# Performance work log

Measured on AMD Instinct MI355X. Metric: run time of the kernel, lower is better.

## Reference

```python
import jax, jax.numpy as jnp
import numpy as np

VDIM, HDIM, B = 128, 512, 512
EPS = 1e-5  # torch LayerNorm default


def _ln(x, g, b):
    m = x.mean(-1, keepdims=True)
    v = ((x - m) ** 2).mean(-1, keepdims=True)
    return (x - m) * jax.lax.rsqrt(v + EPS) * g + b


def setup_inputs() -> dict:
    key = jax.random.key(0)
    ks = jax.random.split(key, 16)
    s = 0.05  # small init so sigmoids/logs stay numerically tame
    d = {}
    d["u"] = jax.random.uniform(ks[0], (VDIM, B), jnp.float32)
    d["q_w1"] = s * jax.random.normal(ks[1], (VDIM, HDIM), jnp.float32)
    d["q_b1"] = jnp.zeros((HDIM,), jnp.float32)
    d["q_g1"] = jnp.ones((HDIM,), jnp.float32)
    d["q_be1"] = jnp.zeros((HDIM,), jnp.float32)
    d["q_w2"] = s * jax.random.normal(ks[2], (HDIM, HDIM), jnp.float32)
    d["q_b2"] = jnp.zeros((HDIM,), jnp.float32)
    d["q_g2"] = jnp.ones((HDIM,), jnp.float32)
    d["q_be2"] = jnp.zeros((HDIM,), jnp.float32)
    d["q_w3"] = s * jax.random.normal(ks[3], (HDIM, HDIM), jnp.float32)
    d["q_b3"] = jnp.zeros((HDIM,), jnp.float32)
    d["q_g3"] = jnp.ones((HDIM,), jnp.float32)
    d["q_be3"] = jnp.zeros((HDIM,), jnp.float32)
    d["q_W"] = 0.01 * jax.random.normal(ks[4], (VDIM, HDIM), jnp.float32)  # per-node output heads
    d["q_bias"] = jnp.zeros((VDIM,), jnp.float32)
    d["q_marg"] = jnp.zeros((VDIM,), jnp.float32)
    d["f_w1"] = s * jax.random.normal(ks[5], (VDIM, HDIM), jnp.float32)
    d["f_b1"] = jnp.zeros((HDIM,), jnp.float32)
    d["f_g1"] = jnp.ones((HDIM,), jnp.float32)
    d["f_be1"] = jnp.zeros((HDIM,), jnp.float32)
    d["f_w2"] = s * jax.random.normal(ks[6], (HDIM, HDIM), jnp.float32)
    d["f_b2"] = jnp.zeros((HDIM,), jnp.float32)
    d["f_g2"] = jnp.ones((HDIM,), jnp.float32)
    d["f_be2"] = jnp.zeros((HDIM,), jnp.float32)
    d["f_w3"] = s * jax.random.normal(ks[7], (HDIM, HDIM), jnp.float32)
    d["f_b3"] = jnp.zeros((HDIM,), jnp.float32)
    d["f_g3"] = jnp.ones((HDIM,), jnp.float32)
    d["f_be3"] = jnp.zeros((HDIM,), jnp.float32)
    d["f_w4"] = s * jax.random.normal(ks[8], (HDIM,), jnp.float32)
    d["f_b4"] = jnp.zeros((1,), jnp.float32)
    d["J"] = 0.1 * jax.random.normal(ks[9], (VDIM, VDIM), jnp.float32)  # Ising couplings for scorer
    d["top_order"] = jnp.arange(VDIM, dtype=jnp.int32)
    d["pa_mask"] = jax.random.randint(ks[10], (VDIM, VDIM), 0, 2, jnp.int32)
    return d


def reference(u, q_w1, q_b1, q_g1, q_be1, q_w2, q_b2, q_g2, q_be2,
              q_w3, q_b3, q_g3, q_be3, q_W, q_bias, q_marg,
              f_w1, f_b1, f_g1, f_be1, f_w2, f_b2, f_g2, f_be2,
              f_w3, f_b3, f_g3, f_be3, f_w4, f_b4, J,
              top_order, pa_mask):
    def qtrunk(V):
        h = jax.nn.relu(_ln(V @ q_w1 + q_b1, q_g1, q_be1))
        h = jax.nn.relu(_ln(h @ q_w2 + q_b2, q_g2, q_be2))
        h = jax.nn.relu(_ln(h @ q_w3 + q_b3, q_g3, q_be3))
        return h  # [B, H]

    def fnet(V):
        h = jax.nn.relu(_ln(V @ f_w1 + f_b1, f_g1, f_be1))
        h = jax.nn.relu(_ln(h @ f_w2 + f_b2, f_g2, f_be2))
        h = jax.nn.relu(_ln(h @ f_w3 + f_b3, f_g3, f_be3))
        return h @ f_w4 + f_b4[0]  # [B]

    # gather per-node quantities in topological order once, outside the scan
    masks = pa_mask[top_order].astype(u.dtype)          # [V, V] parent masks
    Wq = q_W[top_order]                                  # [V, H]
    bq = q_bias[top_order]                               # [V]
    mg = q_marg[top_order]                               # [V]
    oh = jax.nn.one_hot(top_order, VDIM, dtype=u.dtype)  # [V, V]

    def step(V, xs):
        mask_i, Wq_i, bq_i, mg_i, oh_i, u_i = xs
        V_pa = V * mask_i                                # [B, V] parents only
        x = qtrunk(V_pa) @ Wq_i + bq_i                   # [B]
        empty = jnp.abs(V_pa).sum(1) == 0
        p_on = jnp.where(empty, jax.nn.sigmoid(mg_i), jax.nn.sigmoid(x))
        samp = u_i < p_on                                # bernoulli(p_on)
        v_samp = 2.0 * samp.astype(u.dtype) - 1.0
        V_new = V * (1.0 - oh_i) + v_samp[:, None] * oh_i  # scatter into column
        lp = jnp.where(samp, jnp.log(p_on), jnp.log1p(-p_on))
        logF = fnet(jax.lax.stop_gradient(V_new))        # V.clone().detach()
        return V_new, (lp, logF)

    V0 = jnp.zeros((B, VDIM), u.dtype)
    V, (lps, logFs) = jax.lax.scan(step, V0, (masks, Wq, bq, mg, oh, u))
    log_pf = lps.T                                       # [B, V]
    F0 = fnet(V0)                                        # log_flow[:, 0] (alg='db')
    score = jax.lax.stop_gradient(jnp.einsum('bi,ij,bj->b', V, J, V))  # -energy, detached
    # last logF is overwritten by the terminal score, as in the original
    log_flow = jnp.concatenate([F0[:, None], logFs[:-1].T, score[:, None]], axis=1)  # [B, V+1]
    loss = ((log_flow[:, :-1] + log_pf - log_flow[:, 1:]) ** 2).mean(1).mean()
    return V, loss
```

## Files before the change

kernel.cpp:

```cpp
#include <hip/hip_runtime.h>
#include <hip/hip_bf16.h>
#include <math.h>

#define VDIM 128
#define HDIM 512
#define BATCH 512
#define RPB 4
#define NBLK (BATCH / RPB)
#define NWORK 128
#define NT 512
#define NWAVE 8
#define LN_EPS 1e-5f
#define FROWS 32
#define NGRP (BATCH / FROWS)
#define SBPG (FROWS / RPB)

__device__ __forceinline__ float4 f4zero() { return make_float4(0.f, 0.f, 0.f, 0.f); }
__device__ __forceinline__ float4 f4add(float4 a, float4 b) {
    return make_float4(a.x + b.x, a.y + b.y, a.z + b.z, a.w + b.w);
}
__device__ __forceinline__ float4 f4fma(float4 a, float s, float4 c) {
    return make_float4(fmaf(a.x, s, c.x), fmaf(a.y, s, c.y),
                       fmaf(a.z, s, c.z), fmaf(a.w, s, c.w));
}
__device__ __forceinline__ float4 f4scale(float4 a, float s) {
    return make_float4(a.x * s, a.y * s, a.z * s, a.w * s);
}
__device__ __forceinline__ float4 f4sub(float4 a, float4 b) {
    return make_float4(a.x - b.x, a.y - b.y, a.z - b.z, a.w - b.w);
}
__device__ __forceinline__ float f4get(float4 v, int r) {
    return r == 0 ? v.x : r == 1 ? v.y : r == 2 ? v.z : v.w;
}

struct Params {
    const float *u;
    const float *q_w1, *q_b1, *q_g1, *q_be1;
    const float *q_w2, *q_b2, *q_g2, *q_be2;
    const float *q_w3, *q_b3, *q_g3, *q_be3;
    const float *q_W, *q_bias, *q_marg;
    const float *f_w1, *f_b1, *f_g1, *f_be1;
    const float *f_w2, *f_b2, *f_g2, *f_be2;
    const float *f_w3, *f_b3, *f_g3, *f_be3;
    const float *f_w4, *f_b4, *J;
    const int *top_order, *pa_mask;
    int *flag;
    float *V_out, *lp, *lf, *score, *vs, *loss;
};

struct ScanS {
    float4 VT[VDIM];
    float4 VPT[VDIM];
    float4 ATa[HDIM];
    float4 ATb[HDIM];
    float4 part[4][4][128];
    float4 redA[NWAVE], redB[NWAVE];
};
struct WorkS {
    float Vt[VDIM * FROWS];
    float A[HDIM * FROWS];
    int ord[VDIM], invp[VDIM];
    float4 redA[NWAVE], redB[NWAVE];
};
union SMem { ScanS s; WorkS w; };

__device__ __forceinline__ float4 allreduce4_1s(float4 v, float4 *red, int tid) {
#pragma unroll
    for (int off = 1; off < 64; off <<= 1) {
        v.x += __shfl_xor(v.x, off, 64);
        v.y += __shfl_xor(v.y, off, 64);
        v.z += __shfl_xor(v.z, off, 64);
        v.w += __shfl_xor(v.w, off, 64);
    }
    if ((tid & 63) == 0) red[tid >> 6] = v;
    __syncthreads();
    float4 s = red[0];
#pragma unroll
    for (int w = 1; w < NWAVE; ++w) s = f4add(s, red[w]);
    return s;
}

__device__ __forceinline__ float block_reduce1(float v, float *red, int tid) {
#pragma unroll
    for (int off = 1; off < 64; off <<= 1) v += __shfl_xor(v, off, 64);
    if ((tid & 63) == 0) red[tid >> 6] = v;
    __syncthreads();
    float s = 0.f;
#pragma unroll
    for (int w = 0; w < NWAVE; ++w) s += red[w];
    __syncthreads();
    return s;
}

__device__ __forceinline__ void redpair(float4 &a, float4 &b,
                                        float4 *redA, float4 *redB, int tid) {
#pragma unroll
    for (int off = 1; off < 64; off <<= 1) {
        a.x += __shfl_xor(a.x, off, 64); a.y += __shfl_xor(a.y, off, 64);
        a.z += __shfl_xor(a.z, off, 64); a.w += __shfl_xor(a.w, off, 64);
        b.x += __shfl_xor(b.x, off, 64); b.y += __shfl_xor(b.y, off, 64);
        b.z += __shfl_xor(b.z, off, 64); b.w += __shfl_xor(b.w, off, 64);
    }
    int w = tid >> 6;
    if ((tid & 63) == 0) { redA[w] = a; redB[w] = b; }
    __syncthreads();
    int p = w ^ 1;
    a = f4add(redA[w], redA[p]);
    b = f4add(redB[w], redB[p]);
    __syncthreads();
}

template <int K>
__device__ __forceinline__ void gemv_ln_scan(const float4 *__restrict__ inA,
                                             const float *__restrict__ W,
                                             const float *__restrict__ bias,
                                             const float *__restrict__ gam,
                                             const float *__restrict__ bet,
                                             float4 *__restrict__ outA,
                                             ScanS &S, int tid, int ks, int cq,
                                             int myc) {
    constexpr int kc = K / 4;
    constexpr int q4 = kc / 4;
    constexpr int seg = K / 4;
    const float4 *Wp = (const float4 *)W + (size_t)(ks * kc) * (HDIM / 4) + cq;
    const float4 *ap = inA + ks * q4;
    float4 acc0 = f4zero(), acc1 = f4zero(), acc2 = f4zero(), acc3 = f4zero();
#pragma unroll 4
    for (int q = 0; q < q4; ++q) {
        float4 a0 = ap[q];
        float4 a1 = ap[q + seg];
        float4 a2 = ap[q + 2 * seg];
        float4 a3 = ap[q + 3 * seg];
        float4 w0 = Wp[(size_t)(4 * q + 0) * (HDIM / 4)];
        float4 w1 = Wp[(size_t)(4 * q + 1) * (HDIM / 4)];
        float4 w2 = Wp[(size_t)(4 * q + 2) * (HDIM / 4)];
        float4 w3 = Wp[(size_t)(4 * q + 3) * (HDIM / 4)];
        acc0 = f4fma(a0, w0.x, acc0); acc1 = f4fma(a0, w0.y, acc1);
        acc2 = f4fma(a0, w0.z, acc2); acc3 = f4fma(a0, w0.w, acc3);
        acc0 = f4fma(a1, w1.x, acc0); acc1 = f4fma(a1, w1.y, acc1);
        acc2 = f4fma(a1, w1.z, acc2); acc3 = f4fma(a1, w1.w, acc3);
        acc0 = f4fma(a2, w2.x, acc0); acc1 = f4fma(a2, w2.y, acc1);
        acc2 = f4fma(a2, w2.z, acc2); acc3 = f4fma(a2, w2.w, acc3);
        acc0 = f4fma(a3, w3.x, acc0); acc1 = f4fma(a3, w3.y, acc1);
        acc2 = f4fma(a3, w3.z, acc2); acc3 = f4fma(a3, w3.w, acc3);
    }
    S.part[0][ks][cq] = acc0;
    S.part[1][ks][cq] = acc1;
    S.part[2][ks][cq] = acc2;
    S.part[3][ks][cq] = acc3;
    __syncthreads();
    const int j = ks, cb = cq;
    float4 acc = f4add(f4add(S.part[j][0][cb], S.part[j][1][cb]),
                       f4add(S.part[j][2][cb], S.part[j][3][cb]));
    float bc = bias[myc];
    acc.x += bc; acc.y += bc; acc.z += bc; acc.w += bc;
    const float inv = 1.f / (float)HDIM;
    float4 m4 = f4scale(allreduce4_1s(acc, S.redA, tid), inv);
    float4 d = f4sub(acc, m4);
    float4 sq = make_float4(d.x * d.x, d.y * d.y, d.z * d.z, d.w * d.w);
    float4 var = f4scale(allreduce4_1s(sq, S.redB, tid), inv);
    float4 rs;
    rs.x = 1.f / sqrtf(var.x + LN_EPS);
    rs.y = 1.f / sqrtf(var.y + LN_EPS);
    rs.z = 1.f / sqrtf(var.z + LN_EPS);
    rs.w = 1.f / sqrtf(var.w + LN_EPS);
    float gc = gam[myc], ec = bet[myc];
    float4 h;
    h.x = fmaxf(fmaf(d.x * rs.x, gc, ec), 0.f);
    h.y = fmaxf(fmaf(d.y * rs.y, gc, ec), 0.f);
    h.z = fmaxf(fmaf(d.z * rs.z, gc, ec), 0.f);
    h.w = fmaxf(fmaf(d.w * rs.w, gc, ec), 0.f);
    outA[tid] = h;
    __syncthreads();
}

__device__ void scan_role(const Params &P, int bid, ScanS &S) {
    const int tid = threadIdx.x;
    const int ks = tid >> 7;
    const int cq = tid & 127;
    const int myc = 4 * cq + ks;
    const int row0 = bid * RPB;

    if (tid < VDIM) S.VT[tid] = f4zero();
    __syncthreads();

    for (int i = 0; i < VDIM; ++i) {
        const int node = P.top_order[i];

        float4 apv = f4zero();
        if (tid < VDIM) {
            float mk = (float)P.pa_mask[node * VDIM + tid];
            float4 vp = f4scale(S.VT[tid], mk);
            S.VPT[(tid & 3) * 32 + (tid >> 2)] = vp;
            apv = make_float4(fabsf(vp.x), fabsf(vp.y), fabsf(vp.z), fabsf(vp.w));
        }
        float4 asum = allreduce4_1s(apv, S.redB, tid);

        gemv_ln_scan<VDIM>(S.VPT, P.q_w1, P.q_b1, P.q_g1, P.q_be1, S.ATa, S, tid, ks, cq, myc);
        gemv_ln_scan<HDIM>(S.ATa, P.q_w2, P.q_b2, P.q_g2, P.q_be2, S.ATb, S, tid, ks, cq, myc);
        gemv_ln_scan<HDIM>(S.ATb, P.q_w3, P.q_b3, P.q_g3, P.q_be3, S.ATa, S, tid, ks, cq, myc);

        float wq = P.q_W[(size_t)node * HDIM + myc];
        float4 x4 = allreduce4_1s(f4scale(S.ATa[tid], wq), S.redA, tid);

        if (tid < RPB) {
            const int r = tid;
            float asr = f4get(asum, r);
            float xr = f4get(x4, r) + P.q_bias[node];
            float arg = (asr == 0.f) ? P.q_marg[node] : xr;
            float p = 1.f / (1.f + expf(-arg));
            float uv = P.u[i * BATCH + row0 + r];
            bool samp = uv < p;
            float v = samp ? 1.f : -1.f;
            ((float *)&S.VT[node])[r] = v;
            __hip_atomic_store(&P.vs[(size_t)i * BATCH + row0 + r], v,
                               __ATOMIC_RELAXED, __HIP_MEMORY_SCOPE_AGENT);
            P.lp[(size_t)i * BATCH + row0 + r] = samp ? logf(p) : log1pf(-p);
        }
        __syncthreads();
        if (tid == 0) {
            __hip_atomic_store(P.flag + bid, i + 1,
                               __ATOMIC_RELEASE, __HIP_MEMORY_SCOPE_AGENT);
        }
    }

    float4 inner = f4zero();
    if (tid < VDIM) {
#pragma unroll 4
        for (int ii = 0; ii < VDIM; ++ii)
            inner = f4fma(S.VT[ii], P.J[(size_t)ii * VDIM + tid], inner);
        float4 vc = S.VT[tid];
        inner = make_float4(inner.x * vc.x, inner.y * vc.y, inner.z * vc.z, inner.w * vc.w);
    }
    float4 sc4 = allreduce4_1s(inner, S.redA, tid);
    if (tid < RPB) P.score[row0 + tid] = f4get(sc4, tid);
    if (tid < VDIM) {
        float4 v = S.VT[tid];
        P.V_out[(size_t)(row0 + 0) * VDIM + tid] = v.x;
        P.V_out[(size_t)(row0 + 1) * VDIM + tid] = v.y;
        P.V_out[(size_t)(row0 + 2) * VDIM + tid] = v.z;
        P.V_out[(size_t)(row0 + 3) * VDIM + tid] = v.w;
    }
}

template <int K>
__device__ __forceinline__ void flayer512(const float *__restrict__ in,
                                          const float *__restrict__ W,
                                          const float *__restrict__ bias,
                                          const float *__restrict__ gam,
                                          const float *__restrict__ bet,
                                          float *__restrict__ out,
                                          float4 *redA, float4 *redB, int tid) {
    const int rh = tid >> 7;
    const int cq = tid & 127;
    const float4 *Wv = (const float4 *)W + cq;
    float4 accA[4], accB[4];
#pragma unroll
    for (int j = 0; j < 4; ++j) { accA[j] = f4zero(); accB[j] = f4zero(); }
#pragma unroll 4
    for (int k = 0; k < K; ++k) {
        float4 w = Wv[(size_t)k * (HDIM / 4)];
        const float *ip = in + k * FROWS + 8 * rh;
        float4 vA = *(const float4 *)ip;
        float4 vB = *(const float4 *)(ip + 4);
        accA[0] = f4fma(vA, w.x, accA[0]); accB[0] = f4fma(vB, w.x, accB[0]);
        accA[1] = f4fma(vA, w.y, accA[1]); accB[1] = f4fma(vB, w.y, accB[1]);
        accA[2] = f4fma(vA, w.z, accA[2]); accB[2] = f4fma(vB, w.z, accB[2]);
        accA[3] = f4fma(vA, w.w, accA[3]); accB[3] = f4fma(vB, w.w, accB[3]);
    }
    float4 b4 = ((const float4 *)bias)[cq];
    float bb[4] = {b4.x, b4.y, b4.z, b4.w};
#pragma unroll
    for (int j = 0; j < 4; ++j) {
        accA[j].x += bb[j]; accA[j].y += bb[j]; accA[j].z += bb[j]; accA[j].w += bb[j];
        accB[j].x += bb[j]; accB[j].y += bb[j]; accB[j].z += bb[j]; accB[j].w += bb[j];
    }
    const float inv = 1.f / (float)HDIM;
    float4 sA = f4add(f4add(accA[0], accA[1]), f4add(accA[2], accA[3]));
    float4 sB = f4add(f4add(accB[0], accB[1]), f4add(accB[2], accB[3]));
    redpair(sA, sB, redA, redB, tid);
    float4 mA = f4scale(sA, inv), mB = f4scale(sB, inv);
    float4 dA[4], dB[4];
    float4 qA = f4zero(), qB = f4zero();
#pragma unroll
    for (int j = 0; j < 4; ++j) {
        dA[j] = f4sub(accA[j], mA);
        dB[j] = f4sub(accB[j], mB);
        qA.x += dA[j].x * dA[j].x; qA.y += dA[j].y * dA[j].y;
        qA.z += dA[j].z * dA[j].z; qA.w += dA[j].w * dA[j].w;
        qB.x += dB[j].x * dB[j].x; qB.y += dB[j].y * dB[j].y;
        qB.z += dB[j].z * dB[j].z; qB.w += dB[j].w * dB[j].w;
    }
    redpair(qA, qB, redA, redB, tid);
    float4 rsA, rsB;
    rsA.x = 1.f / sqrtf(qA.x * inv + LN_EPS); rsA.y = 1.f / sqrtf(qA.y * inv + LN_EPS);
    rsA.z = 1.f / sqrtf(qA.z * inv + LN_EPS); rsA.w = 1.f / sqrtf(qA.w * inv + LN_EPS);
    rsB.x = 1.f / sqrtf(qB.x * inv + LN_EPS); rsB.y = 1.f / sqrtf(qB.y * inv + LN_EPS);
    rsB.z = 1.f / sqrtf(qB.z * inv + LN_EPS); rsB.w = 1.f / sqrtf(qB.w * inv + LN_EPS);
    float4 g4 = ((const float4 *)gam)[cq];
    float4 e4 = ((const float4 *)bet)[cq];
    float gg[4] = {g4.x, g4.y, g4.z, g4.w};
    float ee[4] = {e4.x, e4.y, e4.z, e4.w};
#pragma unroll
    for (int j = 0; j < 4; ++j) {
        float4 hA, hB;
        hA.x = fmaxf(fmaf(dA[j].x * rsA.x, gg[j], ee[j]), 0.f);
        hA.y = fmaxf(fmaf(dA[j].y * rsA.y, gg[j], ee[j]), 0.f);
        hA.z = fmaxf(fmaf(dA[j].z * rsA.z, gg[j], ee[j]), 0.f);
        hA.w = fmaxf(fmaf(dA[j].w * rsA.w, gg[j], ee[j]), 0.f);
        hB.x = fmaxf(fmaf(dB[j].x * rsB.x, gg[j], ee[j]), 0.f);
        hB.y = fmaxf(fmaf(dB[j].y * rsB.y, gg[j], ee[j]), 0.f);
        hB.z = fmaxf(fmaf(dB[j].z * rsB.z, gg[j], ee[j]), 0.f);
        hB.w = fmaxf(fmaf(dB[j].w * rsB.w, gg[j], ee[j]), 0.f);
        float *op = out + (4 * cq + j) * FROWS + 8 * rh;
        *(float4 *)op = hA;
        *(float4 *)(op + 4) = hB;
    }
    __syncthreads();
}

__device__ void worker_role(const Params &P, int wid, WorkS &S) {
    const int tid = threadIdx.x;
    if (tid < VDIM) S.ord[tid] = P.top_order[tid];
    __syncthreads();
    if (tid < VDIM) S.invp[S.ord[tid]] = tid;
    __syncthreads();
    const int g = wid & (NGRP - 1);
    const int r0 = g * FROWS;

    for (int tile = wid; tile < VDIM * NGRP; tile += NWORK) {
        const int t = tile >> 4;
        if (t == VDIM - 1) continue;
        if (tid < SBPG) {
            const int need = t + 1;
            while (__hip_atomic_load(P.flag + (SBPG * g + tid),
                                     __ATOMIC_RELAXED,
                                     __HIP_MEMORY_SCOPE_AGENT) < need)
                __builtin_amdgcn_s_sleep(4);
        }
        __syncthreads();
        for (int idx = tid; idx < VDIM * FROWS; idx += NT) {
            int k = idx >> 5, rr = idx & (FROWS - 1);
            int s = S.invp[k];
            S.Vt[idx] = (s <= t)
                ? __hip_atomic_load(&P.vs[(size_t)s * BATCH + r0 + rr],
                                    __ATOMIC_RELAXED, __HIP_MEMORY_SCOPE_AGENT)
                : 0.f;
        }
        __syncthreads();

        flayer512<VDIM>(S.Vt, P.f_w1, P.f_b1, P.f_g1, P.f_be1, S.A, S.redA, S.redB, tid);
        flayer512<HDIM>(S.A, P.f_w2, P.f_b2, P.f_g2, P.f_be2, S.A, S.redA, S.redB, tid);
        flayer512<HDIM>(S.A, P.f_w3, P.f_b3, P.f_g3, P.f_be3, S.A, S.redA, S.redB, tid);

        const int rh = tid >> 7, cq = tid & 127;
        float4 w4 = ((const float4 *)P.f_w4)[cq];
        float ww[4] = {w4.x, w4.y, w4.z, w4.w};
        float4 sA = f4zero(), sB = f4zero();
#pragma unroll
        for (int j = 0; j < 4; ++j) {
            const float *ap2 = S.A + (4 * cq + j) * FROWS + 8 * rh;
            float4 vA = *(const float4 *)ap2;
            float4 vB = *(const float4 *)(ap2 + 4);
            sA = f4fma(vA, ww[j], sA);
            sB = f4fma(vB, ww[j], sB);
        }
        redpair(sA, sB, S.redA, S.redB, tid);
        if (cq == 0) {
            float b4v = P.f_b4[0];
            float *dst = P.lf + (size_t)t * BATCH + r0 + 8 * rh;
            dst[0] = sA.x + b4v; dst[1] = sA.y + b4v;
            dst[2] = sA.z + b4v; dst[3] = sA.w + b4v;
            dst[4] = sB.x + b4v; dst[5] = sB.y + b4v;
            dst[6] = sB.z + b4v; dst[7] = sB.w + b4v;
        }
        __syncthreads();
    }
}

__global__ __launch_bounds__(NT) void gfn_main(Params P) {
    __shared__ SMem sm;
    const int xcd = blockIdx.x & 7;
    const int grp = blockIdx.x >> 3;
    if (xcd < 4) scan_role(P, grp * 4 + xcd, sm.s);
    else         worker_role(P, grp * 4 + (xcd - 4), sm.w);
}

__global__ __launch_bounds__(NT) void gfn_loss(Params P) {
    __shared__ float H1[HDIM], H2[HDIM];
    __shared__ float red1[NWAVE];
    const int tid = threadIdx.x;
    const float inv = 1.f / (float)HDIM;

    float z = P.f_b1[tid];
    float m = block_reduce1(z, red1, tid) * inv;
    float d = z - m;
    float var = block_reduce1(d * d, red1, tid) * inv;
    float h = fmaxf(fmaf(d * (1.f / sqrtf(var + LN_EPS)), P.f_g1[tid], P.f_be1[tid]), 0.f);
    H1[tid] = h;
    __syncthreads();

    float acc = 0.f;
    for (int k = 0; k < HDIM; ++k) acc = fmaf(H1[k], P.f_w2[(size_t)k * HDIM + tid], acc);
    z = acc + P.f_b2[tid];
    m = block_reduce1(z, red1, tid) * inv;
    d = z - m;
    var = block_reduce1(d * d, red1, tid) * inv;
    h = fmaxf(fmaf(d * (1.f / sqrtf(var + LN_EPS)), P.f_g2[tid], P.f_be2[tid]), 0.f);
    H2[tid] = h;
    __syncthreads();

    acc = 0.f;
    for (int k = 0; k < HDIM; ++k) acc = fmaf(H2[k], P.f_w3[(size_t)k * HDIM + tid], acc);
    z = acc + P.f_b3[tid];
    m = block_reduce1(z, red1, tid) * inv;
    d = z - m;
    var = block_reduce1(d * d, red1, tid) * inv;
    h = fmaxf(fmaf(d * (1.f / sqrtf(var + LN_EPS)), P.f_g3[tid], P.f_be3[tid]), 0.f);
    float F0 = block_reduce1(h * P.f_w4[tid], red1, tid) + P.f_b4[0];

    const int b = tid;
    float lfp = F0;
    float s = 0.f;
    for (int t = 0; t < VDIM; ++t) {
        float lp = P.lp[(size_t)t * BATCH + b];
        float lfn = (t == VDIM - 1) ? P.score[b] : P.lf[(size_t)t * BATCH + b];
        float dd = lfp + lp - lfn;
        s = fmaf(dd, dd, s);
        lfp = lfn;
    }
    s *= (1.f / (float)VDIM);
    float total = block_reduce1(s, red1, tid) * (1.f / (float)BATCH);
    if (tid == 0) P.loss[0] = total;
}

extern "C" void kernel_launch(void *const *d_in, const int *in_sizes, int n_in,
                              void *d_out, int out_size, void *d_ws, size_t ws_size,
                              hipStream_t stream) {
    Params P;
    P.u     = (const float *)d_in[0];
    P.q_w1  = (const float *)d_in[1];
    P.q_b1  = (const float *)d_in[2];
    P.q_g1  = (const float *)d_in[3];
    P.q_be1 = (const float *)d_in[4];
    P.q_w2  = (const float *)d_in[5];
    P.q_b2  = (const float *)d_in[6];
    P.q_g2  = (const float *)d_in[7];
    P.q_be2 = (const float *)d_in[8];
    P.q_w3  = (const float *)d_in[9];
    P.q_b3  = (const float *)d_in[10];
    P.q_g3  = (const float *)d_in[11];
    P.q_be3 = (const float *)d_in[12];
    P.q_W   = (const float *)d_in[13];
    P.q_bias= (const float *)d_in[14];
    P.q_marg= (const float *)d_in[15];
    P.f_w1  = (const float *)d_in[16];
    P.f_b1  = (const float *)d_in[17];
    P.f_g1  = (const float *)d_in[18];
    P.f_be1 = (const float *)d_in[19];
    P.f_w2  = (const float *)d_in[20];
    P.f_b2  = (const float *)d_in[21];
    P.f_g2  = (const float *)d_in[22];
    P.f_be2 = (const float *)d_in[23];
    P.f_w3  = (const float *)d_in[24];
    P.f_b3  = (const float *)d_in[25];
    P.f_g3  = (const float *)d_in[26];
    P.f_be3 = (const float *)d_in[27];
    P.f_w4  = (const float *)d_in[28];
    P.f_b4  = (const float *)d_in[29];
    P.J     = (const float *)d_in[30];
    P.top_order = (const int *)d_in[31];
    P.pa_mask   = (const int *)d_in[32];

    float *ws = (float *)d_ws;
    P.V_out = (float *)d_out;
    P.loss  = (float *)d_out + (size_t)BATCH * VDIM;
    P.lp    = ws;
    P.lf    = ws + (size_t)VDIM * BATCH;
    P.score = ws + 2 * (size_t)VDIM * BATCH;
    P.vs    = ws + 2 * (size_t)VDIM * BATCH + BATCH;
    P.flag  = (int *)(ws + 3 * (size_t)VDIM * BATCH + BATCH);

    hipMemsetAsync(P.flag, 0, NBLK * sizeof(int), stream);
    gfn_main<<<dim3(NBLK + NWORK), dim3(NT), 0, stream>>>(P);
    gfn_loss<<<dim3(1), dim3(NT), 0, stream>>>(P);
}
```

Before: 3.821 ms.

## Pair scan blocks to split GEMV K dimension and exchange partial sums

Each scan block now handles 8 batch rows instead of 4, and two blocks form a pair that each compute half of the K reduction for every GEMV layer. The halves are exchanged through a double-buffered global scratch area guarded by per-pair flags. This halves the weight traffic per block per row and doubles the rows that share each weight load. The cost is a cross-block spin-wait handshake three times per sequential step, which adds latency on the critical path. Both members redundantly run LayerNorm and sampling, and only member 0 writes the outputs.

```diff
diff --git a/kernel.cpp b/kernel.cpp
--- a/kernel.cpp
+++ b/kernel.cpp
@@ -5,15 +5,15 @@
 #define VDIM 128
 #define HDIM 512
 #define BATCH 512
-#define RPB 4
-#define NBLK (BATCH / RPB)
+#define RPB 8
+#define NPAIR 64
 #define NWORK 128
 #define NT 512
 #define NWAVE 8
 #define LN_EPS 1e-5f
 #define FROWS 32
-#define NGRP (BATCH / FROWS)
-#define SBPG (FROWS / RPB)
+#define NGRP 16
+#define PPG 4
 
 __device__ __forceinline__ float4 f4zero() { return make_float4(0.f, 0.f, 0.f, 0.f); }
 __device__ __forceinline__ float4 f4add(float4 a, float4 b) {
@@ -28,6 +28,9 @@
 }
 __device__ __forceinline__ float4 f4sub(float4 a, float4 b) {
     return make_float4(a.x - b.x, a.y - b.y, a.z - b.z, a.w - b.w);
+}
+__device__ __forceinline__ float4 f4abs(float4 a) {
+    return make_float4(fabsf(a.x), fabsf(a.y), fabsf(a.z), fabsf(a.w));
 }
 __device__ __forceinline__ float f4get(float4 v, int r) {
     return r == 0 ? v.x : r == 1 ? v.y : r == 2 ? v.z : v.w;
@@ -44,17 +47,19 @@
     const float *f_w3, *f_b3, *f_g3, *f_be3;
     const float *f_w4, *f_b4, *J;
     const int *top_order, *pa_mask;
-    int *flag;
+    int *wflag;
+    int *xflag;
+    float *xbuf;
     float *V_out, *lp, *lf, *score, *vs, *loss;
 };
 
 struct ScanS {
-    float4 VT[VDIM];
-    float4 VPT[VDIM];
-    float4 ATa[HDIM];
-    float4 ATb[HDIM];
-    float4 part[4][4][128];
-    float4 redA[NWAVE], redB[NWAVE];
+    float4 VT[VDIM][2];
+    float4 VPT[VDIM][2];
+    float4 ATa[HDIM][2];
+    float4 ATb[HDIM][2];
+    float4 part[4][4][128][2];
+    float4 redA[NWAVE][2], redB[NWAVE][2];
 };
 struct WorkS {
     float Vt[VDIM * FROWS];
@@ -64,36 +69,8 @@
 };
 union SMem { ScanS s; WorkS w; };
 
-__device__ __forceinline__ float4 allreduce4_1s(float4 v, float4 *red, int tid) {
-#pragma unroll
-    for (int off = 1; off < 64; off <<= 1) {
-        v.x += __shfl_xor(v.x, off, 64);
-        v.y += __shfl_xor(v.y, off, 64);
-        v.z += __shfl_xor(v.z, off, 64);
-        v.w += __shfl_xor(v.w, off, 64);
-    }
-    if ((tid & 63) == 0) red[tid >> 6] = v;
-    __syncthreads();
-    float4 s = red[0];
-#pragma unroll
-    for (int w = 1; w < NWAVE; ++w) s = f4add(s, red[w]);
-    return s;
-}
-
-__device__ __forceinline__ float block_reduce1(float v, float *red, int tid) {
-#pragma unroll
-    for (int off = 1; off < 64; off <<= 1) v += __shfl_xor(v, off, 64);
-    if ((tid & 63) == 0) red[tid >> 6] = v;
-    __syncthreads();
-    float s = 0.f;
-#pragma unroll
-    for (int w = 0; w < NWAVE; ++w) s += red[w];
-    __syncthreads();
-    return s;
-}
-
-__device__ __forceinline__ void redpair(float4 &a, float4 &b,
-                                        float4 *redA, float4 *redB, int tid) {
+__device__ __forceinline__ void allreduce2_1s(float4 &a, float4 &b,
+                                              float4 (*red)[2], int tid) {
 #pragma unroll
     for (int off = 1; off < 64; off <<= 1) {
         a.x += __shfl_xor(a.x, off, 64); a.y += __shfl_xor(a.y, off, 64);
@@ -101,6 +78,35 @@
         b.x += __shfl_xor(b.x, off, 64); b.y += __shfl_xor(b.y, off, 64);
         b.z += __shfl_xor(b.z, off, 64); b.w += __shfl_xor(b.w, off, 64);
     }
+    if ((tid & 63) == 0) { red[tid >> 6][0] = a; red[tid >> 6][1] = b; }
+    __syncthreads();
+    float4 sa = red[0][0], sb = red[0][1];
+#pragma unroll
+    for (int w = 1; w < NWAVE; ++w) { sa = f4add(sa, red[w][0]); sb = f4add(sb, red[w][1]); }
+    a = sa; b = sb;
+}
+
+__device__ __forceinline__ float block_reduce1(float v, float *red, int tid) {
+#pragma unroll
+    for (int off = 1; off < 64; off <<= 1) v += __shfl_xor(v, off, 64);
+    if ((tid & 63) == 0) red[tid >> 6] = v;
+    __syncthreads();
+    float s = 0.f;
+#pragma unroll
+    for (int w = 0; w < NWAVE; ++w) s += red[w];
+    __syncthreads();
+    return s;
+}
+
+__device__ __forceinline__ void redpair(float4 &a, float4 &b,
+                                        float4 *redA, float4 *redB, int tid) {
+#pragma unroll
+    for (int off = 1; off < 64; off <<= 1) {
+        a.x += __shfl_xor(a.x, off, 64); a.y += __shfl_xor(a.y, off, 64);
+        a.z += __shfl_xor(a.z, off, 64); a.w += __shfl_xor(a.w, off, 64);
+        b.x += __shfl_xor(b.x, off, 64); b.y += __shfl_xor(b.y, off, 64);
+        b.z += __shfl_xor(b.z, off, 64); b.w += __shfl_xor(b.w, off, 64);
+    }
     int w = tid >> 6;
     if ((tid & 63) == 0) { redA[w] = a; redB[w] = b; }
     __syncthreads();
@@ -111,135 +117,217 @@
 }
 
 template <int K>
-__device__ __forceinline__ void gemv_ln_scan(const float4 *__restrict__ inA,
-                                             const float *__restrict__ W,
-                                             const float *__restrict__ bias,
-                                             const float *__restrict__ gam,
-                                             const float *__restrict__ bet,
-                                             float4 *__restrict__ outA,
-                                             ScanS &S, int tid, int ks, int cq,
-                                             int myc) {
-    constexpr int kc = K / 4;
+__device__ __forceinline__ void gemv8(const float4 (*__restrict__ inA)[2],
+                                      const float *__restrict__ W,
+                                      const float *__restrict__ bias,
+                                      const float *__restrict__ gam,
+                                      const float *__restrict__ bet,
+                                      float4 (*__restrict__ outA)[2],
+                                      ScanS &S, int tid, int ks, int cq, int myc,
+                                      int member, float *xb_me2, float *xb_pt2,
+                                      int *xf_me, int *xf_pt, int tag) {
+    constexpr int half = K / 2;
+    constexpr int kc = K / 8;
     constexpr int q4 = kc / 4;
     constexpr int seg = K / 4;
-    const float4 *Wp = (const float4 *)W + (size_t)(ks * kc) * (HDIM / 4) + cq;
-    const float4 *ap = inA + ks * q4;
-    float4 acc0 = f4zero(), acc1 = f4zero(), acc2 = f4zero(), acc3 = f4zero();
-#pragma unroll 4
+    const int mOff = member * half;
+    const float4 *Wp = (const float4 *)W + (size_t)(mOff + ks * kc) * (HDIM / 4) + cq;
+    const float4 (*ap)[2] = inA + (mOff >> 2) + ks * q4;
+
+    float4 l0 = f4zero(), l1 = f4zero(), l2 = f4zero(), l3 = f4zero();
+    float4 h0 = f4zero(), h1 = f4zero(), h2 = f4zero(), h3 = f4zero();
+#pragma unroll 2
     for (int q = 0; q < q4; ++q) {
-        float4 a0 = ap[q];
-        float4 a1 = ap[q + seg];
-        float4 a2 = ap[q + 2 * seg];
-        float4 a3 = ap[q + 3 * seg];
+        float4 a0l = ap[q][0],           a0h = ap[q][1];
+        float4 a1l = ap[q + seg][0],     a1h = ap[q + seg][1];
+        float4 a2l = ap[q + 2 * seg][0], a2h = ap[q + 2 * seg][1];
+        float4 a3l = ap[q + 3 * seg][0], a3h = ap[q + 3 * seg][1];
         float4 w0 = Wp[(size_t)(4 * q + 0) * (HDIM / 4)];
         float4 w1 = Wp[(size_t)(4 * q + 1) * (HDIM / 4)];
         float4 w2 = Wp[(size_t)(4 * q + 2) * (HDIM / 4)];
         float4 w3 = Wp[(size_t)(4 * q + 3) * (HDIM / 4)];
-        acc0 = f4fma(a0, w0.x, acc0); acc1 = f4fma(a0, w0.y, acc1);
-        acc2 = f4fma(a0, w0.z, acc2); acc3 = f4fma(a0, w0.w, acc3);
-        acc0 = f4fma(a1, w1.x, acc0); acc1 = f4fma(a1, w1.y, acc1);
-        acc2 = f4fma(a1, w1.z, acc2); acc3 = f4fma(a1, w1.w, acc3);
-        acc0 = f4fma(a2, w2.x, acc0); acc1 = f4fma(a2, w2.y, acc1);
-        acc2 = f4fma(a2, w2.z, acc2); acc3 = f4fma(a2, w2.w, acc3);
-        acc0 = f4fma(a3, w3.x, acc0); acc1 = f4fma(a3, w3.y, acc1);
-        acc2 = f4fma(a3, w3.z, acc2); acc3 = f4fma(a3, w3.w, acc3);
-    }
-    S.part[0][ks][cq] = acc0;
-    S.part[1][ks][cq] = acc1;
-    S.part[2][ks][cq] = acc2;
-    S.part[3][ks][cq] = acc3;
-    __syncthreads();
+        l0 = f4fma(a0l, w0.x, l0); h0 = f4fma(a0h, w0.x, h0);
+        l1 = f4fma(a0l, w0.y, l1); h1 = f4fma(a0h, w0.y, h1);
+        l2 = f4fma(a0l, w0.z, l2); h2 = f4fma(a0h, w0.z, h2);
+        l3 = f4fma(a0l, w0.w, l3); h3 = f4fma(a0h, w0.w, h3);
+        l0 = f4fma(a1l, w1.x, l0); h0 = f4fma(a1h, w1.x, h0);
+        l1 = f4fma(a1l, w1.y, l1); h1 = f4fma(a1h, w1.y, h1);
+        l2 = f4fma(a1l, w1.z, l2); h2 = f4fma(a1h, w1.z, h2);
+        l3 = f4fma(a1l, w1.w, l3); h3 = f4fma(a1h, w1.w, h3);
+        l0 = f4fma(a2l, w2.x, l0); h0 = f4fma(a2h, w2.x, h0);
+        l1 = f4fma(a2l, w2.y, l1); h1 = f4fma(a2h, w2.y, h1);
+        l2 = f4fma(a2l, w2.z, l2); h2 = f4fma(a2h, w2.z, h2);
+        l3 = f4fma(a2l, w2.w, l3); h3 = f4fma(a2h, w2.w, h3);
+        l0 = f4fma(a3l, w3.x, l0); h0 = f4fma(a3h, w3.x, h0);
+        l1 = f4fma(a3l, w3.y, l1); h1 = f4fma(a3h, w3.y, h1);
+        l2 = f4fma(a3l, w3.z, l2); h2 = f4fma(a3h, w3.z, h2);
+        l3 = f4fma(a3l, w3.w, l3); h3 = f4fma(a3h, w3.w, h3);
+    }
+    S.part[0][ks][cq][0] = l0; S.part[0][ks][cq][1] = h0;
+    S.part[1][ks][cq][0] = l1; S.part[1][ks][cq][1] = h1;
+    S.part[2][ks][cq][0] = l2; S.part[2][ks][cq][1] = h2;
+    S.part[3][ks][cq][0] = l3; S.part[3][ks][cq][1] = h3;
+    __syncthreads();
+
     const int j = ks, cb = cq;
-    float4 acc = f4add(f4add(S.part[j][0][cb], S.part[j][1][cb]),
-                       f4add(S.part[j][2][cb], S.part[j][3][cb]));
+    float4 lo = f4add(f4add(S.part[j][0][cb][0], S.part[j][1][cb][0]),
+                      f4add(S.part[j][2][cb][0], S.part[j][3][cb][0]));
+    float4 hi = f4add(f4add(S.part[j][0][cb][1], S.part[j][1][cb][1]),
+                      f4add(S.part[j][2][cb][1], S.part[j][3][cb][1]));
+
+    const int slot = (tag - 1) & 1;
+    float *dst = xb_me2 + (size_t)slot * 4096 + (size_t)myc * 8;
+    __hip_atomic_store(dst + 0, lo.x, __ATOMIC_RELAXED, __HIP_MEMORY_SCOPE_AGENT);
+    __hip_atomic_store(dst + 1, lo.y, __ATOMIC_RELAXED, __HIP_MEMORY_SCOPE_AGENT);
+    __hip_atomic_store(dst + 2, lo.z, __ATOMIC_RELAXED, __HIP_MEMORY_SCOPE_AGENT);
+    __hip_atomic_store(dst + 3, lo.w, __ATOMIC_RELAXED, __HIP_MEMORY_SCOPE_AGENT);
+    __hip_atomic_store(dst + 4, hi.x, __ATOMIC_RELAXED, __HIP_MEMORY_SCOPE_AGENT);
+    __hip_atomic_store(dst + 5, hi.y, __ATOMIC_RELAXED, __HIP_MEMORY_SCOPE_AGENT);
+    __hip_atomic_store(dst + 6, hi.z, __ATOMIC_RELAXED, __HIP_MEMORY_SCOPE_AGENT);
+    __hip_atomic_store(dst + 7, hi.w, __ATOMIC_RELAXED, __HIP_MEMORY_SCOPE_AGENT);
+    __syncthreads();
+    if (tid == 0) {
+        __hip_atomic_store(xf_me, tag, __ATOMIC_RELEASE, __HIP_MEMORY_SCOPE_AGENT);
+        while (__hip_atomic_load(xf_pt, __ATOMIC_RELAXED, __HIP_MEMORY_SCOPE_AGENT) < tag)
+            __builtin_amdgcn_s_sleep(1);
+    }
+    __syncthreads();
+    const float *src = xb_pt2 + (size_t)slot * 4096 + (size_t)myc * 8;
+    lo.x += __hip_atomic_load(src + 0, __ATOMIC_RELAXED, __HIP_MEMORY_SCOPE_AGENT);
+    lo.y += __hip_atomic_load(src + 1, __ATOMIC_RELAXED, __HIP_MEMORY_SCOPE_AGENT);
+    lo.z += __hip_atomic_load(src + 2, __ATOMIC_RELAXED, __HIP_MEMORY_SCOPE_AGENT);
+    lo.w += __hip_atomic_load(src + 3, __ATOMIC_RELAXED, __HIP_MEMORY_SCOPE_AGENT);
+    hi.x += __hip_atomic_load(src + 4, __ATOMIC_RELAXED, __HIP_MEMORY_SCOPE_AGENT);
+    hi.y += __hip_atomic_load(src + 5, __ATOMIC_RELAXED, __HIP_MEMORY_SCOPE_AGENT);
+    hi.z += __hip_atomic_load(src + 6, __ATOMIC_RELAXED, __HIP_MEMORY_SCOPE_AGENT);
+    hi.w += __hip_atomic_load(src + 7, __ATOMIC_RELAXED, __HIP_MEMORY_SCOPE_AGENT);
+
     float bc = bias[myc];
-    acc.x += bc; acc.y += bc; acc.z += bc; acc.w += bc;
+    lo.x += bc; lo.y += bc; lo.z += bc; lo.w += bc;
+    hi.x += bc; hi.y += bc; hi.z += bc; hi.w += bc;
+
     const float inv = 1.f / (float)HDIM;
-    float4 m4 = f4scale(allreduce4_1s(acc, S.redA, tid), inv);
-    float4 d = f4sub(acc, m4);
-    float4 sq = make_float4(d.x * d.x, d.y * d.y, d.z * d.z, d.w * d.w);
-    float4 var = f4scale(allreduce4_1s(sq, S.redB, tid), inv);
-    float4 rs;
-    rs.x = 1.f / sqrtf(var.x + LN_EPS);
-    rs.y = 1.f / sqrtf(var.y + LN_EPS);
-    rs.z = 1.f / sqrtf(var.z + LN_EPS);
-    rs.w = 1.f / sqrtf(var.w + LN_EPS);
+    float4 sl = lo, sh = hi;
+    allreduce2_1s(sl, sh, S.redA, tid);
+    float4 ml = f4scale(sl, inv), mh = f4scale(sh, inv);
+    float4 dl = f4sub(lo, ml), dh = f4sub(hi, mh);
+    float4 ql = make_float4(dl.x * dl.x, dl.y * dl.y, dl.z * dl.z, dl.w * dl.w);
+    float4 qh = make_float4(dh.x * dh.x, dh.y * dh.y, dh.z * dh.z, dh.w * dh.w);
+    allreduce2_1s(ql, qh, S.redB, tid);
+    float4 rl, rh;
+    rl.x = 1.f / sqrtf(ql.x * inv + LN_EPS); rl.y = 1.f / sqrtf(ql.y * inv + LN_EPS);
+    rl.z = 1.f / sqrtf(ql.z * inv + LN_EPS); rl.w = 1.f / sqrtf(ql.w * inv + LN_EPS);
+    rh.x = 1.f / sqrtf(qh.x * inv + LN_EPS); rh.y = 1.f / sqrtf(qh.y * inv + LN_EPS);
+    rh.z = 1.f / sqrtf(qh.z * inv + LN_EPS); rh.w = 1.f / sqrtf(qh.w * inv + LN_EPS);
     float gc = gam[myc], ec = bet[myc];
-    float4 h;
-    h.x = fmaxf(fmaf(d.x * rs.x, gc, ec), 0.f);
-    h.y = fmaxf(fmaf(d.y * rs.y, gc, ec), 0.f);
-    h.z = fmaxf(fmaf(d.z * rs.z, gc, ec), 0.f);
-    h.w = fmaxf(fmaf(d.w * rs.w, gc, ec), 0.f);
-    outA[tid] = h;
-    __syncthreads();
-}
-
-__device__ void scan_role(const Params &P, int bid, ScanS &S) {
+    float4 ol, oh;
+    ol.x = fmaxf(fmaf(dl.x * rl.x, gc, ec), 0.f);
+    ol.y = fmaxf(fmaf(dl.y * rl.y, gc, ec), 0.f);
+    ol.z = fmaxf(fmaf(dl.z * rl.z, gc, ec), 0.f);
+    ol.w = fmaxf(fmaf(dl.w * rl.w, gc, ec), 0.f);
+    oh.x = fmaxf(fmaf(dh.x * rh.x, gc, ec), 0.f);
+    oh.y = fmaxf(fmaf(dh.y * rh.y, gc, ec), 0.f);
+    oh.z = fmaxf(fmaf(dh.z * rh.z, gc, ec), 0.f);
+    oh.w = fmaxf(fmaf(dh.w * rh.w, gc, ec), 0.f);
+    outA[tid][0] = ol;
+    outA[tid][1] = oh;
+    __syncthreads();
+}
+
+__device__ void scan_role(const Params &P, int scanid, ScanS &S) {
     const int tid = threadIdx.x;
     const int ks = tid >> 7;
     const int cq = tid & 127;
     const int myc = 4 * cq + ks;
-    const int row0 = bid * RPB;
-
-    if (tid < VDIM) S.VT[tid] = f4zero();
+    const int pair = scanid >> 1;
+    const int member = scanid & 1;
+    const int row0 = pair * RPB;
+
+    int *xf_me = P.xflag + pair * 2 + member;
+    int *xf_pt = P.xflag + pair * 2 + (member ^ 1);
+    float *xb_me2 = P.xbuf + (size_t)(pair * 2 + member) * 2 * 4096;
+    float *xb_pt2 = P.xbuf + (size_t)(pair * 2 + (member ^ 1)) * 2 * 4096;
+
+    if (tid < VDIM) { S.VT[tid][0] = f4zero(); S.VT[tid][1] = f4zero(); }
     __syncthreads();
 
     for (int i = 0; i < VDIM; ++i) {
         const int node = P.top_order[i];
 
-        float4 apv = f4zero();
+        float4 apl = f4zero(), aph = f4zero();
         if (tid < VDIM) {
             float mk = (float)P.pa_mask[node * VDIM + tid];
-            float4 vp = f4scale(S.VT[tid], mk);
-            S.VPT[(tid & 3) * 32 + (tid >> 2)] = vp;
-            apv = make_float4(fabsf(vp.x), fabsf(vp.y), fabsf(vp.z), fabsf(vp.w));
-        }
-        float4 asum = allreduce4_1s(apv, S.redB, tid);
-
-        gemv_ln_scan<VDIM>(S.VPT, P.q_w1, P.q_b1, P.q_g1, P.q_be1, S.ATa, S, tid, ks, cq, myc);
-        gemv_ln_scan<HDIM>(S.ATa, P.q_w2, P.q_b2, P.q_g2, P.q_be2, S.ATb, S, tid, ks, cq, myc);
-        gemv_ln_scan<HDIM>(S.ATb, P.q_w3, P.q_b3, P.q_g3, P.q_be3, S.ATa, S, tid, ks, cq, myc);
+            float4 vl = f4scale(S.VT[tid][0], mk);
+            float4 vh = f4scale(S.VT[tid][1], mk);
+            int st = (tid & 3) * 32 + (tid >> 2);
+            S.VPT[st][0] = vl; S.VPT[st][1] = vh;
+            apl = f4abs(vl); aph = f4abs(vh);
+        }
+        allreduce2_1s(apl, aph, S.redB, tid);
+        float4 asumL = apl, asumH = aph;
+
+        const int tau = i * 3;
+        gemv8<VDIM>(S.VPT, P.q_w1, P.q_b1, P.q_g1, P.q_be1, S.ATa, S, tid, ks, cq, myc,
+                    member, xb_me2, xb_pt2, xf_me, xf_pt, tau + 1);
+        gemv8<HDIM>(S.ATa, P.q_w2, P.q_b2, P.q_g2, P.q_be2, S.ATb, S, tid, ks, cq, myc,
+                    member, xb_me2, xb_pt2, xf_me, xf_pt, tau + 2);
+        gemv8<HDIM>(S.ATb, P.q_w3, P.q_b3, P.q_g3, P.q_be3, S.ATa, S, tid, ks, cq, myc,
+                    member, xb_me2, xb_pt2, xf_me, xf_pt, tau + 3);
 
         float wq = P.q_W[(size_t)node * HDIM + myc];
-        float4 x4 = allreduce4_1s(f4scale(S.ATa[tid], wq), S.redA, tid);
+        float4 xl = f4scale(S.ATa[tid][0], wq);
+        float4 xh = f4scale(S.ATa[tid][1], wq);
+        allreduce2_1s(xl, xh, S.redA, tid);
 
         if (tid < RPB) {
             const int r = tid;
-            float asr = f4get(asum, r);
-            float xr = f4get(x4, r) + P.q_bias[node];
+            float asr = (r < 4) ? f4get(asumL, r) : f4get(asumH, r - 4);
+            float xr = ((r < 4) ? f4get(xl, r) : f4get(xh, r - 4)) + P.q_bias[node];
             float arg = (asr == 0.f) ? P.q_marg[node] : xr;
             float p = 1.f / (1.f + expf(-arg));
             float uv = P.u[i * BATCH + row0 + r];
             bool samp = uv < p;
             float v = samp ? 1.f : -1.f;
-            ((float *)&S.VT[node])[r] = v;
-            __hip_atomic_store(&P.vs[(size_t)i * BATCH + row0 + r], v,
-                               __ATOMIC_RELAXED, __HIP_MEMORY_SCOPE_AGENT);
-            P.lp[(size_t)i * BATCH + row0 + r] = samp ? logf(p) : log1pf(-p);
+            ((float *)&S.VT[node][r >> 2])[r & 3] = v;
+            if (member == 0) {
+                __hip_atomic_store(&P.vs[(size_t)i * BATCH + row0 + r], v,
+                                   __ATOMIC_RELAXED, __HIP_MEMORY_SCOPE_AGENT);
+                P.lp[(size_t)i * BATCH + row0 + r] = samp ? logf(p) : log1pf(-p);
+            }
         }
         __syncthreads();
-        if (tid == 0) {
-            __hip_atomic_store(P.flag + bid, i + 1,
+        if (member == 0 && tid == 0)
+            __hip_atomic_store(P.wflag + pair, i + 1,
                                __ATOMIC_RELEASE, __HIP_MEMORY_SCOPE_AGENT);
-        }
-    }
-
-    float4 inner = f4zero();
+    }
+
+    float4 il = f4zero(), ih = f4zero();
     if (tid < VDIM) {
 #pragma unroll 4
-        for (int ii = 0; ii < VDIM; ++ii)
-            inner = f4fma(S.VT[ii], P.J[(size_t)ii * VDIM + tid], inner);
-        float4 vc = S.VT[tid];
-        inner = make_float4(inner.x * vc.x, inner.y * vc.y, inner.z * vc.z, inner.w * vc.w);
-    }
-    float4 sc4 = allreduce4_1s(inner, S.redA, tid);
-    if (tid < RPB) P.score[row0 + tid] = f4get(sc4, tid);
-    if (tid < VDIM) {
-        float4 v = S.VT[tid];
-        P.V_out[(size_t)(row0 + 0) * VDIM + tid] = v.x;
-        P.V_out[(size_t)(row0 + 1) * VDIM + tid] = v.y;
-        P.V_out[(size_t)(row0 + 2) * VDIM + tid] = v.z;
-        P.V_out[(size_t)(row0 + 3) * VDIM + tid] = v.w;
+        for (int ii = 0; ii < VDIM; ++ii) {
+            float jv = P.J[(size_t)ii * VDIM + tid];
+            il = f4fma(S.VT[ii][0], jv, il);
+            ih = f4fma(S.VT[ii][1], jv, ih);
+        }
+        float4 vl = S.VT[tid][0], vh = S.VT[tid][1];
+        il = make_float4(il.x * vl.x, il.y * vl.y, il.z * vl.z, il.w * vl.w);
+        ih = make_float4(ih.x * vh.x, ih.y * vh.y, ih.z * vh.z, ih.w * vh.w);
+    }
+    allreduce2_1s(il, ih, S.redA, tid);
+    if (member == 0) {
+        if (tid < RPB)
+            P.score[row0 + tid] = (tid < 4) ? f4get(il, tid) : f4get(ih, tid - 4);
+        if (tid < VDIM) {
+            float4 vl = S.VT[tid][0], vh = S.VT[tid][1];
+            P.V_out[(size_t)(row0 + 0) * VDIM + tid] = vl.x;
+            P.V_out[(size_t)(row0 + 1) * VDIM + tid] = vl.y;
+            P.V_out[(size_t)(row0 + 2) * VDIM + tid] = vl.z;
+            P.V_out[(size_t)(row0 + 3) * VDIM + tid] = vl.w;
+            P.V_out[(size_t)(row0 + 4) * VDIM + tid] = vh.x;
+            P.V_out[(size_t)(row0 + 5) * VDIM + tid] = vh.y;
+            P.V_out[(size_t)(row0 + 6) * VDIM + tid] = vh.z;
+            P.V_out[(size_t)(row0 + 7) * VDIM + tid] = vh.w;
+        }
     }
 }
 
@@ -331,9 +419,9 @@
     for (int tile = wid; tile < VDIM * NGRP; tile += NWORK) {
         const int t = tile >> 4;
         if (t == VDIM - 1) continue;
-        if (tid < SBPG) {
+        if (tid < PPG) {
             const int need = t + 1;
-            while (__hip_atomic_load(P.flag + (SBPG * g + tid),
+            while (__hip_atomic_load(P.wflag + (PPG * g + tid),
                                      __ATOMIC_RELAXED,
                                      __HIP_MEMORY_SCOPE_AGENT) < need)
                 __builtin_amdgcn_s_sleep(4);
@@ -382,8 +470,12 @@
     __shared__ SMem sm;
     const int xcd = blockIdx.x & 7;
     const int grp = blockIdx.x >> 3;
-    if (xcd < 4) scan_role(P, grp * 4 + xcd, sm.s);
-    else         worker_role(P, grp * 4 + (xcd - 4), sm.w);
+    if (xcd < 4) {
+        const int pair = (grp >> 1) * 4 + xcd;
+        scan_role(P, pair * 2 + (grp & 1), sm.s);
+    } else {
+        worker_role(P, grp * 4 + (xcd - 4), sm.w);
+    }
 }
 
 __global__ __launch_bounds__(NT) void gfn_loss(Params P) {
@@ -479,9 +571,11 @@
     P.lf    = ws + (size_t)VDIM * BATCH;
     P.score = ws + 2 * (size_t)VDIM * BATCH;
     P.vs    = ws + 2 * (size_t)VDIM * BATCH + BATCH;
-    P.flag  = (int *)(ws + 3 * (size_t)VDIM * BATCH + BATCH);
-
-    hipMemsetAsync(P.flag, 0, NBLK * sizeof(int), stream);
-    gfn_main<<<dim3(NBLK + NWORK), dim3(NT), 0, stream>>>(P);
+    P.wflag = (int *)(ws + 3 * (size_t)VDIM * BATCH + BATCH);
+    P.xflag = P.wflag + NPAIR;
+    P.xbuf  = (float *)(P.xflag + 2 * NPAIR);
+
+    hipMemsetAsync(P.wflag, 0, 3 * NPAIR * sizeof(int), stream);
+    gfn_main<<<dim3(NPAIR * 2 + NWORK), dim3(NT), 0, stream>>>(P);
     gfn_loss<<<dim3(1), dim3(NT), 0, stream>>>(P);
 }
```

After: 10.15 ms. 166% more time.

## Cut per-step barriers in scan: fused LN moments, precomputed empty flags, fused parent prep

Applied to the files above, without the earlier changes.

LayerNorm now reduces sum and sum-of-squares in a single block allreduce instead of two sequential ones, which removes one barrier round per layer. The empty-parent test is precomputed once per node at kernel start from the mask and topological order, which removes the per-step abs-sum reduction. The masked parent vector for the next step is built in the same phase that writes the sampled value, so each of the 128 sequential steps has fewer syncs. The one-pass variance formula is clamped at zero but can lose some precision compared with the two-pass form.

```diff
diff --git a/kernel.cpp b/kernel.cpp
--- a/kernel.cpp
+++ b/kernel.cpp
@@ -12,8 +12,8 @@
 #define NWAVE 8
 #define LN_EPS 1e-5f
 #define FROWS 32
-#define NGRP (BATCH / FROWS)
-#define SBPG (FROWS / RPB)
+#define NGRP 16
+#define SBPG 8
 
 __device__ __forceinline__ float4 f4zero() { return make_float4(0.f, 0.f, 0.f, 0.f); }
 __device__ __forceinline__ float4 f4add(float4 a, float4 b) {
@@ -44,7 +44,7 @@
     const float *f_w3, *f_b3, *f_g3, *f_be3;
     const float *f_w4, *f_b4, *J;
     const int *top_order, *pa_mask;
-    int *flag;
+    int *wflag;
     float *V_out, *lp, *lf, *score, *vs, *loss;
 };
 
@@ -54,7 +54,10 @@
     float4 ATa[HDIM];
     float4 ATb[HDIM];
     float4 part[4][4][128];
-    float4 redA[NWAVE], redB[NWAVE];
+    float4 red2[NWAVE][2];
+    float4 redH[NWAVE];
+    int ord[VDIM];
+    int emptyb[VDIM];
 };
 struct WorkS {
     float Vt[VDIM * FROWS];
@@ -78,6 +81,23 @@
 #pragma unroll
     for (int w = 1; w < NWAVE; ++w) s = f4add(s, red[w]);
     return s;
+}
+
+__device__ __forceinline__ void allreduce2_1s(float4 &a, float4 &b,
+                                              float4 (*red)[2], int tid) {
+#pragma unroll
+    for (int off = 1; off < 64; off <<= 1) {
+        a.x += __shfl_xor(a.x, off, 64); a.y += __shfl_xor(a.y, off, 64);
+        a.z += __shfl_xor(a.z, off, 64); a.w += __shfl_xor(a.w, off, 64);
+        b.x += __shfl_xor(b.x, off, 64); b.y += __shfl_xor(b.y, off, 64);
+        b.z += __shfl_xor(b.z, off, 64); b.w += __shfl_xor(b.w, off, 64);
+    }
+    if ((tid & 63) == 0) { red[tid >> 6][0] = a; red[tid >> 6][1] = b; }
+    __syncthreads();
+    float4 sa = red[0][0], sb = red[0][1];
+#pragma unroll
+    for (int w = 1; w < NWAVE; ++w) { sa = f4add(sa, red[w][0]); sb = f4add(sb, red[w][1]); }
+    a = sa; b = sb;
 }
 
 __device__ __forceinline__ float block_reduce1(float v, float *red, int tid) {
@@ -150,20 +170,26 @@
     S.part[3][ks][cq] = acc3;
     __syncthreads();
     const int j = ks, cb = cq;
-    float4 acc = f4add(f4add(S.part[j][0][cb], S.part[j][1][cb]),
-                       f4add(S.part[j][2][cb], S.part[j][3][cb]));
+    float4 z = f4add(f4add(S.part[j][0][cb], S.part[j][1][cb]),
+                     f4add(S.part[j][2][cb], S.part[j][3][cb]));
     float bc = bias[myc];
-    acc.x += bc; acc.y += bc; acc.z += bc; acc.w += bc;
+    z.x += bc; z.y += bc; z.z += bc; z.w += bc;
     const float inv = 1.f / (float)HDIM;
-    float4 m4 = f4scale(allreduce4_1s(acc, S.redA, tid), inv);
-    float4 d = f4sub(acc, m4);
-    float4 sq = make_float4(d.x * d.x, d.y * d.y, d.z * d.z, d.w * d.w);
-    float4 var = f4scale(allreduce4_1s(sq, S.redB, tid), inv);
+    float4 s1 = z;
+    float4 s2 = make_float4(z.x * z.x, z.y * z.y, z.z * z.z, z.w * z.w);
+    allreduce2_1s(s1, s2, S.red2, tid);
+    float4 m = f4scale(s1, inv);
+    float4 e2 = f4scale(s2, inv);
+    float4 var = make_float4(fmaxf(e2.x - m.x * m.x, 0.f),
+                             fmaxf(e2.y - m.y * m.y, 0.f),
+                             fmaxf(e2.z - m.z * m.z, 0.f),
+                             fmaxf(e2.w - m.w * m.w, 0.f));
     float4 rs;
     rs.x = 1.f / sqrtf(var.x + LN_EPS);
     rs.y = 1.f / sqrtf(var.y + LN_EPS);
     rs.z = 1.f / sqrtf(var.z + LN_EPS);
     rs.w = 1.f / sqrtf(var.w + LN_EPS);
+    float4 d = f4sub(z, m);
     float gc = gam[myc], ec = bet[myc];
     float4 h;
     h.x = fmaxf(fmaf(d.x * rs.x, gc, ec), 0.f);
@@ -181,46 +207,64 @@
     const int myc = 4 * cq + ks;
     const int row0 = bid * RPB;
 
-    if (tid < VDIM) S.VT[tid] = f4zero();
+    if (tid < VDIM) { S.VT[tid] = f4zero(); S.ord[tid] = P.top_order[tid]; }
+    __syncthreads();
+    if (tid < VDIM) {
+        int nd = S.ord[tid];
+        int mm = 0;
+        for (int jj = 0; jj < tid; ++jj) mm |= P.pa_mask[nd * VDIM + S.ord[jj]];
+        S.emptyb[tid] = (mm == 0);
+        S.VPT[(tid & 3) * 32 + (tid >> 2)] = f4zero();
+    }
     __syncthreads();
 
     for (int i = 0; i < VDIM; ++i) {
-        const int node = P.top_order[i];
-
-        float4 apv = f4zero();
-        if (tid < VDIM) {
-            float mk = (float)P.pa_mask[node * VDIM + tid];
-            float4 vp = f4scale(S.VT[tid], mk);
-            S.VPT[(tid & 3) * 32 + (tid >> 2)] = vp;
-            apv = make_float4(fabsf(vp.x), fabsf(vp.y), fabsf(vp.z), fabsf(vp.w));
-        }
-        float4 asum = allreduce4_1s(apv, S.redB, tid);
+        const int node = S.ord[i];
 
         gemv_ln_scan<VDIM>(S.VPT, P.q_w1, P.q_b1, P.q_g1, P.q_be1, S.ATa, S, tid, ks, cq, myc);
         gemv_ln_scan<HDIM>(S.ATa, P.q_w2, P.q_b2, P.q_g2, P.q_be2, S.ATb, S, tid, ks, cq, myc);
         gemv_ln_scan<HDIM>(S.ATb, P.q_w3, P.q_b3, P.q_g3, P.q_be3, S.ATa, S, tid, ks, cq, myc);
 
         float wq = P.q_W[(size_t)node * HDIM + myc];
-        float4 x4 = allreduce4_1s(f4scale(S.ATa[tid], wq), S.redA, tid);
-
-        if (tid < RPB) {
-            const int r = tid;
-            float asr = f4get(asum, r);
-            float xr = f4get(x4, r) + P.q_bias[node];
-            float arg = (asr == 0.f) ? P.q_marg[node] : xr;
-            float p = 1.f / (1.f + expf(-arg));
-            float uv = P.u[i * BATCH + row0 + r];
-            bool samp = uv < p;
-            float v = samp ? 1.f : -1.f;
-            ((float *)&S.VT[node])[r] = v;
-            __hip_atomic_store(&P.vs[(size_t)i * BATCH + row0 + r], v,
-                               __ATOMIC_RELAXED, __HIP_MEMORY_SCOPE_AGENT);
-            P.lp[(size_t)i * BATCH + row0 + r] = samp ? logf(p) : log1pf(-p);
-        }
-        __syncthreads();
-        if (tid == 0) {
-            __hip_atomic_store(P.flag + bid, i + 1,
-                               __ATOMIC_RELEASE, __HIP_MEMORY_SCOPE_AGENT);
+        float4 x4 = allreduce4_1s(f4scale(S.ATa[tid], wq), S.redH, tid);
+
+        {
+            const bool empty = (S.emptyb[i] != 0);
+            const float qb = P.q_bias[node];
+            const float mg = P.q_marg[node];
+            float a0 = empty ? mg : x4.x + qb;
+            float a1 = empty ? mg : x4.y + qb;
+            float a2 = empty ? mg : x4.z + qb;
+            float a3 = empty ? mg : x4.w + qb;
+            float4 pv = make_float4(1.f / (1.f + expf(-a0)), 1.f / (1.f + expf(-a1)),
+                                    1.f / (1.f + expf(-a2)), 1.f / (1.f + expf(-a3)));
+            float4 uv = *(const float4 *)(P.u + (size_t)i * BATCH + row0);
+            float4 newv = make_float4(uv.x < pv.x ? 1.f : -1.f,
+                                      uv.y < pv.y ? 1.f : -1.f,
+                                      uv.z < pv.z ? 1.f : -1.f,
+                                      uv.w < pv.w ? 1.f : -1.f);
+            if (tid < VDIM) {
+                float mk = 0.f;
+                if (i + 1 < VDIM) {
+                    int nodeN = S.ord[i + 1];
+                    mk = (float)P.pa_mask[nodeN * VDIM + tid];
+                }
+                float4 vk = S.VT[tid];
+                if (tid == node) { vk = newv; S.VT[tid] = newv; }
+                S.VPT[(tid & 3) * 32 + (tid >> 2)] = f4scale(vk, mk);
+            }
+            if (tid < RPB) {
+                float pr = f4get(pv, tid);
+                float vr = f4get(newv, tid);
+                __hip_atomic_store(&P.vs[(size_t)i * BATCH + row0 + tid], vr,
+                                   __ATOMIC_RELAXED, __HIP_MEMORY_SCOPE_AGENT);
+                P.lp[(size_t)i * BATCH + row0 + tid] =
+                    (vr > 0.f) ? logf(pr) : log1pf(-pr);
+            }
+            __syncthreads();
+            if (tid == 0)
+                __hip_atomic_store(P.wflag + bid, i + 1,
+                                   __ATOMIC_RELEASE, __HIP_MEMORY_SCOPE_AGENT);
         }
     }
 
@@ -232,7 +276,7 @@
         float4 vc = S.VT[tid];
         inner = make_float4(inner.x * vc.x, inner.y * vc.y, inner.z * vc.z, inner.w * vc.w);
     }
-    float4 sc4 = allreduce4_1s(inner, S.redA, tid);
+    float4 sc4 = allreduce4_1s(inner, S.redH, tid);
     if (tid < RPB) P.score[row0 + tid] = f4get(sc4, tid);
     if (tid < VDIM) {
         float4 v = S.VT[tid];
@@ -333,7 +377,7 @@
         if (t == VDIM - 1) continue;
         if (tid < SBPG) {
             const int need = t + 1;
-            while (__hip_atomic_load(P.flag + (SBPG * g + tid),
+            while (__hip_atomic_load(P.wflag + (SBPG * g + tid),
                                      __ATOMIC_RELAXED,
                                      __HIP_MEMORY_SCOPE_AGENT) < need)
                 __builtin_amdgcn_s_sleep(4);
@@ -479,9 +523,9 @@
     P.lf    = ws + (size_t)VDIM * BATCH;
     P.score = ws + 2 * (size_t)VDIM * BATCH;
     P.vs    = ws + 2 * (size_t)VDIM * BATCH + BATCH;
-    P.flag  = (int *)(ws + 3 * (size_t)VDIM * BATCH + BATCH);
-
-    hipMemsetAsync(P.flag, 0, NBLK * sizeof(int), stream);
+    P.wflag = (int *)(ws + 3 * (size_t)VDIM * BATCH + BATCH);
+
+    hipMemsetAsync(P.wflag, 0, NBLK * sizeof(int), stream);
     gfn_main<<<dim3(NBLK + NWORK), dim3(NT), 0, stream>>>(P);
     gfn_loss<<<dim3(1), dim3(NT), 0, stream>>>(P);
 }
```

Result: no change. 3.843 ms (+0.6%).
